# Performance work log

Hardware: AMD Instinct MI355X
Metric: run time of the kernel (lower is better)

The kernel has to match this reference:

```python
import jax, jax.numpy as jnp
import numpy as np
from jax import lax

B = 32
NUM_CLASSES = 80
NUM_ANCHORS = 3
IMG_SIZE = 320
STRIDES = (8, 16, 32)
TOPK = 1000
CONF_THRESH = 0.05
NMS_THRESH = 0.6
EPS = 1e-10

ANCHOR_SIZES = np.array([[16, 16], [32, 32], [64, 48],
                         [64, 64], [96, 96], [128, 96],
                         [128, 128], [192, 160], [256, 256]],
                        dtype=np.float32).reshape(3, NUM_ANCHORS, 2)


def _build_anchors():
    # mirrors YOWOv3.generate_anchors
    boxes, strides = [], []
    for lvl, s in enumerate(STRIDES):
        f = IMG_SIZE // s
        ys, xs = np.meshgrid(np.arange(f), np.arange(f), indexing='ij')
        xy = np.stack([xs, ys], axis=-1).astype(np.float32).reshape(-1, 1, 2)
        xy = np.repeat(xy, NUM_ANCHORS, axis=1) * s            # [f*f, A, 2]
        wh = np.broadcast_to(ANCHOR_SIZES[lvl], (f * f, NUM_ANCHORS, 2))
        boxes.append(np.concatenate([xy, wh], axis=-1).reshape(-1, 4))
        strides.append(np.full(f * f * NUM_ANCHORS, s, dtype=np.float32))
    return np.concatenate(boxes, 0), np.concatenate(strides, 0)


def setup_inputs() -> dict:
    key = jax.random.key(0)
    k1, k2, k3 = jax.random.split(key, 3)
    anchors_np, stride_np = _build_anchors()
    M = anchors_np.shape[0]  # 6300
    conf_pred = jax.random.normal(k1, (B, M, 1), dtype=jnp.float32)
    cls_pred = jax.random.normal(k2, (B, M, NUM_CLASSES), dtype=jnp.float32) * 2.0
    reg_pred = jax.random.normal(k3, (B, M, 4), dtype=jnp.float32) * 0.5
    return {
        'conf_pred': conf_pred,
        'cls_pred': cls_pred,
        'reg_pred': reg_pred,
        'anchors': jnp.asarray(anchors_np),
        'stride_map': jnp.asarray(stride_np),
    }


def _decode_boxes(anchors, stride_map, reg_pred):
    # anchors [M,4] (cx, cy, w, h) in pixels; reg_pred [B,M,4]
    ctr = anchors[None, :, :2] + jax.nn.sigmoid(reg_pred[..., :2]) * stride_map[None, :, None]
    wh = anchors[None, :, 2:] * jnp.exp(reg_pred[..., 2:])
    return jnp.concatenate([ctr - 0.5 * wh, ctr + 0.5 * wh], axis=-1)  # [B,M,4] x1y1x2y2


def _nms_keep(boxes, scores, labels):
    # boxes [K,4] sorted by descending score; per-class greedy NMS -> bool keep [K]
    x1, y1, x2, y2 = boxes[:, 0], boxes[:, 1], boxes[:, 2], boxes[:, 3]
    areas = (x2 - x1) * (y2 - y1)
    xx1 = jnp.maximum(x1[:, None], x1[None, :])
    yy1 = jnp.maximum(y1[:, None], y1[None, :])
    xx2 = jnp.minimum(x2[:, None], x2[None, :])
    yy2 = jnp.minimum(y2[:, None], y2[None, :])
    inter = jnp.maximum(EPS, xx2 - xx1) * jnp.maximum(EPS, yy2 - yy1)
    union = jnp.maximum(areas[:, None] + areas[None, :] - inter, EPS)
    iou = inter / union
    suppress = (iou > NMS_THRESH) & (labels[:, None] == labels[None, :])
    keep0 = scores >= CONF_THRESH
    idxs = jnp.arange(boxes.shape[0])

    def body(i, keep):
        # if box i is kept, suppress all later same-class boxes with iou > thresh
        return keep & ~(keep[i] & suppress[i] & (idxs > i))

    return lax.fori_loop(0, boxes.shape[0], body, keep0)


def reference(conf_pred, cls_pred, reg_pred, anchors, stride_map):
    box_pred = _decode_boxes(anchors, stride_map, reg_pred)              # [B,M,4]
    joint = jax.nn.sigmoid(conf_pred) * jax.nn.softmax(cls_pred, -1)     # [B,M,C]
    scores = jnp.max(joint, axis=-1)                                     # [B,M]
    labels = jnp.argmax(joint, axis=-1)                                  # [B,M]

    top_scores, top_idx = lax.top_k(scores, TOPK)                        # sorted desc
    top_labels = jnp.take_along_axis(labels, top_idx, axis=1)
    top_boxes = jnp.take_along_axis(box_pred, top_idx[..., None], axis=1)
    top_boxes = jnp.clip(top_boxes / IMG_SIZE, 0.0, 1.0)                 # [B,K,4]

    keep = jax.vmap(_nms_keep)(top_boxes, top_scores, top_labels)        # [B,K] bool
    return top_scores, top_labels, top_boxes, keep
```

## Files before the change

### kernel.cpp

```cpp
#include <hip/hip_runtime.h>
#include <stdint.h>

#define NB 32
#define NM 6300
#define NC 80
#define NTOP 1000
#define NPAD 1024
#define NCAND 2048
#define NBINS 4096
#define BDT 1024

static constexpr float IMGSZ   = 320.0f;
static constexpr float CONF_TH = 0.05f;
static constexpr float NMS_TH  = 0.6f;
static constexpr float EPSF    = 1e-10f;

static constexpr size_t OFF_SCORES = 0;
static constexpr size_t OFF_LABELS = OFF_SCORES + (size_t)NB * NM * 4;
static constexpr size_t OFF_NBOX   = OFF_LABELS + (size_t)NB * NM * 4;
static constexpr size_t OFF_NLAB   = OFF_NBOX   + (size_t)NB * NPAD * 16;
static constexpr size_t OFF_SUP    = ((OFF_NLAB + (size_t)NB * NPAD * 4) + 1023) & ~(size_t)1023;

__global__ __launch_bounds__(256) void k_score(const float* __restrict__ conf,
                                               const float* __restrict__ cls,
                                               float* __restrict__ scores,
                                               int* __restrict__ labels) {
#pragma clang fp contract(off)
    int t = blockIdx.x * blockDim.x + threadIdx.x;
    int a = t >> 4;
    int l = t & 15;
    if (a >= NB * NM) return;
    const float* row = cls + (size_t)a * NC;

    float v[5];
#pragma unroll
    for (int k = 0; k < 5; ++k) v[k] = row[l + 16 * k];

    float bv = v[0];
    int bi = l;
#pragma unroll
    for (int k = 1; k < 5; ++k) {
        int c = l + 16 * k;
        if (v[k] > bv) { bv = v[k]; bi = c; }
    }
#pragma unroll
    for (int m = 1; m < 16; m <<= 1) {
        float ov = __shfl_xor(bv, m, 16);
        int   oi = __shfl_xor(bi, m, 16);
        if (ov > bv || (ov == bv && oi < bi)) { bv = ov; bi = oi; }
    }
    float s = 0.0f;
#pragma unroll
    for (int k = 0; k < 5; ++k) s += expf(v[k] - bv);
#pragma unroll
    for (int m = 1; m < 16; m <<= 1) s += __shfl_xor(s, m, 16);

    if (l == 0) {
        float cf  = conf[a];
        float sig = 1.0f / (1.0f + expf(-cf));
        float inv = 1.0f / s;
        scores[a] = sig * inv;
        labels[a] = bi;
    }
}

__global__ __launch_bounds__(BDT) void k_topk(const float* __restrict__ scores,
                                              const int* __restrict__ labels,
                                              const float* __restrict__ reg,
                                              const float* __restrict__ anchors,
                                              const float* __restrict__ stridemap,
                                              float* __restrict__ out_scores,
                                              float* __restrict__ out_labels,
                                              float* __restrict__ out_boxes,
                                              float* __restrict__ nbox,
                                              int* __restrict__ nlab) {
#pragma clang fp contract(off)
    __shared__ uint32_t hist[NBINS];
    __shared__ uint64_t key[NCAND];
    __shared__ int scnt;
    __shared__ int sT;
    int b = blockIdx.x, tid = threadIdx.x;
    const float* sb = scores + (size_t)b * NM;

    for (int i = tid; i < NBINS; i += BDT) hist[i] = 0;
    for (int i = tid; i < NCAND; i += BDT) key[i] = 0;
    if (tid == 0) scnt = 0;
    __syncthreads();

    for (int i = tid; i < NM; i += BDT)
        atomicAdd(&hist[__float_as_uint(sb[i]) >> 20], 1u);
    __syncthreads();

    if (tid < 64) {
        int l = tid;
        uint32_t q = 0;
        for (int i = 0; i < 64; ++i) q += hist[l * 64 + i];
        uint32_t s = q;
        for (int off = 1; off < 64; off <<= 1) {
            uint32_t o = __shfl_down(s, off);
            if (l + off < 64) s += o;
        }
        uint64_t m = __ballot(s >= (uint32_t)NTOP);
        int c = 63 - __clzll(m);
        uint32_t sc_ = __shfl(s, c);
        uint32_t qc  = __shfl(q, c);
        uint32_t tail = sc_ - qc;
        uint32_t v = hist[c * 64 + l];
        uint32_t s2 = v;
        for (int off = 1; off < 64; off <<= 1) {
            uint32_t o = __shfl_down(s2, off);
            if (l + off < 64) s2 += o;
        }
        uint64_t m2 = __ballot(s2 + tail >= (uint32_t)NTOP);
        int T = c * 64 + (63 - __clzll(m2));
        if (l == 0) sT = T;
    }
    __syncthreads();

    uint32_t T = (uint32_t)sT;
    int lane = tid & 63;
    for (int i = tid; i < NM; i += BDT) {
        uint32_t bits = __float_as_uint(sb[i]);
        bool pred = (bits >> 20) >= T;
        uint64_t mask = __ballot(pred);
        if (pred) {
            int leader = __ffsll((unsigned long long)mask) - 1;
            int prefix = __popcll(mask & ((1ull << lane) - 1));
            int base = 0;
            if (lane == leader) base = atomicAdd(&scnt, (int)__popcll(mask));
            base = __shfl(base, leader);
            int pos = base + prefix;
            if (pos < NCAND)
                key[pos] = ((uint64_t)bits << 32) | (uint32_t)(~(uint32_t)i);
        }
    }
    __syncthreads();

    uint64_t e0 = key[tid];
    uint64_t e1 = key[tid + 1024];

#pragma unroll
    for (int kk = 2; kk <= NCAND; kk <<= 1) {
#pragma unroll
        for (int j = kk >> 1; j > 0; j >>= 1) {
            if (j == 1024) {
                uint64_t mx = (e0 >= e1) ? e0 : e1;
                uint64_t mn = (e0 >= e1) ? e1 : e0;
                e0 = mx; e1 = mn;
            } else if (j >= 64) {
                __syncthreads();
                key[tid] = e0; key[tid + 1024] = e1;
                __syncthreads();
                uint64_t o0 = key[tid ^ j];
                uint64_t o1 = key[(tid + 1024) ^ j];
                bool lo  = ((tid & j) == 0);
                bool up0 = ((tid & kk) == 0);
                bool up1 = (((tid + 1024) & kk) == 0);
                e0 = (lo == up0) ? ((e0 >= o0) ? e0 : o0) : ((e0 >= o0) ? o0 : e0);
                e1 = (lo == up1) ? ((e1 >= o1) ? e1 : o1) : ((e1 >= o1) ? o1 : e1);
            } else {
                uint64_t o0 = __shfl_xor((unsigned long long)e0, j);
                uint64_t o1 = __shfl_xor((unsigned long long)e1, j);
                bool lo  = ((lane & j) == 0);
                bool up0 = ((tid & kk) == 0);
                bool up1 = (((tid + 1024) & kk) == 0);
                e0 = (lo == up0) ? ((e0 >= o0) ? e0 : o0) : ((e0 >= o0) ? o0 : e0);
                e1 = (lo == up1) ? ((e1 >= o1) ? e1 : o1) : ((e1 >= o1) ? o1 : e1);
            }
        }
    }

    if (tid < NTOP) {
        uint32_t sbits = (uint32_t)(e0 >> 32);
        int idx = (int)(~(uint32_t)e0);
        out_scores[b * NTOP + tid] = __uint_as_float(sbits);
        int lab = labels[(size_t)b * NM + idx];
        out_labels[b * NTOP + tid] = (float)lab;

        const float* rg = reg + ((size_t)b * NM + idx) * 4;
        float rx = rg[0], ry = rg[1], rw = rg[2], rh = rg[3];
        const float* an = anchors + (size_t)idx * 4;
        float ax = an[0], ay = an[1], aw = an[2], ah = an[3];
        float st = stridemap[idx];

        float sx = 1.0f / (1.0f + expf(-rx));
        float sy = 1.0f / (1.0f + expf(-ry));
        float cx = ax + sx * st;
        float cy = ay + sy * st;
        float w  = aw * expf(rw);
        float h  = ah * expf(rh);
        float x1 = cx - 0.5f * w, y1 = cy - 0.5f * h;
        float x2 = cx + 0.5f * w, y2 = cy + 0.5f * h;

        float nx1 = fminf(fmaxf(x1 / IMGSZ, 0.0f), 1.0f);
        float ny1 = fminf(fmaxf(y1 / IMGSZ, 0.0f), 1.0f);
        float nx2 = fminf(fmaxf(x2 / IMGSZ, 0.0f), 1.0f);
        float ny2 = fminf(fmaxf(y2 / IMGSZ, 0.0f), 1.0f);

        float4 bx = make_float4(nx1, ny1, nx2, ny2);
        ((float4*)out_boxes)[b * NTOP + tid] = bx;
        ((float4*)nbox)[b * NPAD + tid]      = bx;
        nlab[b * NPAD + tid] = lab;
    }
}

__global__ __launch_bounds__(64) void k_supmat(const float* __restrict__ nbox,
                                               const int* __restrict__ nlab,
                                               uint64_t* __restrict__ sup) {
#pragma clang fp contract(off)
    int b = blockIdx.y;
    int t = blockIdx.x;
    int tj = (int)((sqrtf(8.0f * (float)t + 1.0f) - 1.0f) * 0.5f);
    while ((tj + 1) * (tj + 2) / 2 <= t) ++tj;
    while (tj * (tj + 1) / 2 > t) --tj;
    int ti = t - tj * (tj + 1) / 2;

    int lane = threadIdx.x;
    int j = tj * 64 + lane;

    float4 cj = ((const float4*)nbox)[b * NPAD + j];
    float  aj = (cj.z - cj.x) * (cj.w - cj.y);
    int    lj = nlab[b * NPAD + j];
    bool   jv = (j < NTOP);

    float4 ri = ((const float4*)nbox)[b * NPAD + ti * 64 + lane];
    float  ar = (ri.z - ri.x) * (ri.w - ri.y);
    int    rl = nlab[b * NPAD + ti * 64 + lane];

    uint32_t lobits = 0, hibits = 0;
#pragma unroll
    for (int ii = 0; ii < 64; ++ii) {
        float bix = __shfl(ri.x, ii);
        float biy = __shfl(ri.y, ii);
        float biz = __shfl(ri.z, ii);
        float biw = __shfl(ri.w, ii);
        float aiv = __shfl(ar,   ii);
        int   liv = __shfl(rl,   ii);
        int   ig  = ti * 64 + ii;
        float xx1 = fmaxf(bix, cj.x);
        float yy1 = fmaxf(biy, cj.y);
        float xx2 = fminf(biz, cj.z);
        float yy2 = fminf(biw, cj.w);
        float inter = fmaxf(EPSF, xx2 - xx1) * fmaxf(EPSF, yy2 - yy1);
        float uni   = fmaxf(aiv + aj - inter, EPSF);
        float iou   = inter / uni;
        bool pred = (ig < j) && (ig < NTOP) && jv && (liv == lj) && (iou > NMS_TH);
        if (ii < 32) lobits |= (pred ? (1u << ii) : 0u);
        else         hibits |= (pred ? (1u << (ii - 32)) : 0u);
    }
    sup[(((size_t)b * 16 + tj) * 16 + ti) * 64 + lane] =
        ((uint64_t)hibits << 32) | (uint64_t)lobits;
}

__global__ __launch_bounds__(1024) void k_nms(const float* __restrict__ out_scores,
                                              const uint64_t* __restrict__ sup,
                                              float* __restrict__ out_keep) {
    __shared__ uint64_t Kw[16];
    int b    = blockIdx.x;
    int w    = threadIdx.x >> 6;
    int lane = threadIdx.x & 63;
    const uint64_t* supb = sup + (size_t)b * 16 * 16 * 64;

    uint64_t wrow[16];
#pragma unroll
    for (int ti = 0; ti < 16; ++ti)
        wrow[ti] = (ti <= w) ? supb[((size_t)w * 16 + ti) * 64 + lane] : 0ULL;

    int pos = w * 64 + lane;
    bool k0 = (pos < NTOP) && (out_scores[b * NTOP + pos] >= CONF_TH);

    uint64_t ext = 0;
#pragma unroll
    for (int s = 0; s < 16; ++s) {
        if (w == s) {
            bool cand = k0 && (ext == 0ULL);
            uint64_t wself = wrow[s];
            uint64_t alive = __ballot(cand);
            for (int it = 0; it < 64; ++it) {
                bool dead = (wself & alive) != 0ULL;
                uint64_t na = __ballot(cand && !dead);
                if (na == alive) break;
                alive = na;
            }
            if (lane == 0) Kw[s] = alive;
            if (pos < NTOP)
                out_keep[b * NTOP + pos] = ((alive >> lane) & 1ULL) ? 1.0f : 0.0f;
        }
        __syncthreads();
        if (w > s) ext |= wrow[s] & Kw[s];
    }
}

extern "C" void kernel_launch(void* const* d_in, const int* in_sizes, int n_in,
                              void* d_out, int out_size, void* d_ws, size_t ws_size,
                              hipStream_t stream) {
    const float* conf = (const float*)d_in[0];
    const float* cls  = (const float*)d_in[1];
    const float* reg  = (const float*)d_in[2];
    const float* anch = (const float*)d_in[3];
    const float* strm = (const float*)d_in[4];

    float* out        = (float*)d_out;
    float* out_scores = out;
    float* out_labels = out + NB * NTOP;
    float* out_boxes  = out + 2 * NB * NTOP;
    float* out_keep   = out + 2 * NB * NTOP + NB * NTOP * 4;

    char* ws = (char*)d_ws;
    float*    scores = (float*)(ws + OFF_SCORES);
    int*      labels = (int*)(ws + OFF_LABELS);
    float*    nbox   = (float*)(ws + OFF_NBOX);
    int*      nlab   = (int*)(ws + OFF_NLAB);
    uint64_t* sup    = (uint64_t*)(ws + OFF_SUP);

    k_score<<<(NB * NM * 16) / 256, 256, 0, stream>>>(conf, cls, scores, labels);
    k_topk<<<NB, BDT, 0, stream>>>(scores, labels, reg, anch, strm,
                                   out_scores, out_labels, out_boxes, nbox, nlab);
    k_supmat<<<dim3(136, NB), 64, 0, stream>>>(nbox, nlab, sup);
    k_nms<<<NB, 1024, 0, stream>>>(out_scores, sup, out_keep);
}
```

Measured before the change: 73.58 us.

## Split suppression-matrix tile across four wavefronts using ballot-built bitmasks

The suppression-matrix kernel now uses 256 threads per 64x64 tile instead of 64. Each of the four wavefronts handles 16 of the 64 j columns. Lanes index the i rows, and each column's 64-bit mask comes from a wavefront ballot rather than per-lane bit accumulation. The aim is to cut per-thread serial work and raise occupancy for this small kernel, at the cost of more threads, redundant loads per wave, and only 16 active stores per wave.

```diff
diff --git a/kernel.cpp b/kernel.cpp
--- a/kernel.cpp
+++ b/kernel.cpp
@@ -204,9 +204,9 @@
     }
 }
 
-__global__ __launch_bounds__(64) void k_supmat(const float* __restrict__ nbox,
-                                               const int* __restrict__ nlab,
-                                               uint64_t* __restrict__ sup) {
+__global__ __launch_bounds__(256) void k_supmat(const float* __restrict__ nbox,
+                                                const int* __restrict__ nlab,
+                                                uint64_t* __restrict__ sup) {
 #pragma clang fp contract(off)
     int b = blockIdx.y;
     int t = blockIdx.x;
@@ -215,41 +215,43 @@
     while (tj * (tj + 1) / 2 > t) --tj;
     int ti = t - tj * (tj + 1) / 2;
 
-    int lane = threadIdx.x;
+    int lane = threadIdx.x & 63;
+    int w    = threadIdx.x >> 6;
+
+    int i = ti * 64 + lane;
     int j = tj * 64 + lane;
 
-    float4 cj = ((const float4*)nbox)[b * NPAD + j];
-    float  aj = (cj.z - cj.x) * (cj.w - cj.y);
+    float4 bi = ((const float4*)nbox)[b * NPAD + i];
+    float  ai = (bi.z - bi.x) * (bi.w - bi.y);
+    int    li = nlab[b * NPAD + i];
+    float4 bj = ((const float4*)nbox)[b * NPAD + j];
     int    lj = nlab[b * NPAD + j];
-    bool   jv = (j < NTOP);
-
-    float4 ri = ((const float4*)nbox)[b * NPAD + ti * 64 + lane];
-    float  ar = (ri.z - ri.x) * (ri.w - ri.y);
-    int    rl = nlab[b * NPAD + ti * 64 + lane];
-
-    uint32_t lobits = 0, hibits = 0;
-#pragma unroll
-    for (int ii = 0; ii < 64; ++ii) {
-        float bix = __shfl(ri.x, ii);
-        float biy = __shfl(ri.y, ii);
-        float biz = __shfl(ri.z, ii);
-        float biw = __shfl(ri.w, ii);
-        float aiv = __shfl(ar,   ii);
-        int   liv = __shfl(rl,   ii);
-        int   ig  = ti * 64 + ii;
-        float xx1 = fmaxf(bix, cj.x);
-        float yy1 = fmaxf(biy, cj.y);
-        float xx2 = fminf(biz, cj.z);
-        float yy2 = fminf(biw, cj.w);
+    bool   iv = (i < NTOP);
+
+    uint64_t mybits = 0;
+#pragma unroll
+    for (int u = 0; u < 16; ++u) {
+        int jj = (w << 4) | u;
+        float bjx = __shfl(bj.x, jj);
+        float bjy = __shfl(bj.y, jj);
+        float bjz = __shfl(bj.z, jj);
+        float bjw = __shfl(bj.w, jj);
+        int   ljv = __shfl(lj, jj);
+        float ajv = (bjz - bjx) * (bjw - bjy);
+        int   jg  = tj * 64 + jj;
+        float xx1 = fmaxf(bi.x, bjx);
+        float yy1 = fmaxf(bi.y, bjy);
+        float xx2 = fminf(bi.z, bjz);
+        float yy2 = fminf(bi.w, bjw);
         float inter = fmaxf(EPSF, xx2 - xx1) * fmaxf(EPSF, yy2 - yy1);
-        float uni   = fmaxf(aiv + aj - inter, EPSF);
+        float uni   = fmaxf(ai + ajv - inter, EPSF);
         float iou   = inter / uni;
-        bool pred = (ig < j) && (ig < NTOP) && jv && (liv == lj) && (iou > NMS_TH);
-        if (ii < 32) lobits |= (pred ? (1u << ii) : 0u);
-        else         hibits |= (pred ? (1u << (ii - 32)) : 0u);
-    }
-    sup[(((size_t)b * 16 + tj) * 16 + ti) * 64 + lane] =
-        ((uint64_t)hibits << 32) | (uint64_t)lobits;
+        bool pred = (i < jg) && iv && (jg < NTOP) && (li == ljv) && (iou > NMS_TH);
+        uint64_t bal = __ballot(pred);
+        if (lane == jj) mybits = bal;
+    }
+    if ((lane >> 4) == w)
+        sup[(((size_t)b * 16 + tj) * 16 + ti) * 64 + lane] = mybits;
 }
 
 __global__ __launch_bounds__(1024) void k_nms(const float* __restrict__ out_scores,
@@ -316,6 +318,6 @@
     k_score<<<(NB * NM * 16) / 256, 256, 0, stream>>>(conf, cls, scores, labels);
     k_topk<<<NB, BDT, 0, stream>>>(scores, labels, reg, anch, strm,
                                    out_scores, out_labels, out_boxes, nbox, nlab);
-    k_supmat<<<dim3(136, NB), 64, 0, stream>>>(nbox, nlab, sup);
+    k_supmat<<<dim3(136, NB), 256, 0, stream>>>(nbox, nlab, sup);
     k_nms<<<NB, 1024, 0, stream>>>(out_scores, sup, out_keep);
 }
```

Measured after the change: 67.73 us. 1.09x faster.
